# Performance work log

Measured on AMD Instinct MI355X. Metric: run time of the kernel, lower is better.

## Reference

```python
import jax, jax.numpy as jnp
import numpy as np

D = 2048
N_HEADS = 16
N_KV = 4
HEAD_DIM = D // N_HEADS  # 128
N_REP = N_HEADS // N_KV  # 4
B, S = 2, 2048


def setup_inputs() -> dict:
    key = jax.random.key(0)
    ks = jax.random.split(key, 5)
    scale = 0.02
    return {
        "x": jax.random.normal(ks[0], (B, S, D), dtype=jnp.float32),
        "wq": jax.random.normal(ks[1], (D, N_HEADS * HEAD_DIM), dtype=jnp.float32) * scale,
        "wk": jax.random.normal(ks[2], (D, N_KV * HEAD_DIM), dtype=jnp.float32) * scale,
        "wv": jax.random.normal(ks[3], (D, N_KV * HEAD_DIM), dtype=jnp.float32) * scale,
        "wo": jax.random.normal(ks[4], (N_HEADS * HEAD_DIM, D), dtype=jnp.float32) * scale,
    }


def reference(x, wq, wk, wv, wo):
    b, s, _ = x.shape
    # projections
    xq = (x @ wq).reshape(b, s, N_HEADS, HEAD_DIM)
    xk = (x @ wk).reshape(b, s, N_KV, HEAD_DIM)
    xv = (x @ wv).reshape(b, s, N_KV, HEAD_DIM)
    # GQA: group queries per kv head -> [b, n_kv, n_rep, s, d]
    xq = xq.transpose(0, 2, 1, 3).reshape(b, N_KV, N_REP, s, HEAD_DIM)
    xk = xk.transpose(0, 2, 1, 3)  # [b, n_kv, s, d]
    xv = xv.transpose(0, 2, 1, 3)
    scale = 1.0 / jnp.sqrt(jnp.asarray(HEAD_DIM, dtype=x.dtype))
    scores = jnp.einsum('bkrqd,bkvd->bkrqv', xq, xk) * scale  # [b,n_kv,n_rep,s,s]
    causal = jnp.triu(jnp.ones((s, s), dtype=bool), k=1)
    scores = jnp.where(causal, jnp.asarray(-jnp.inf, dtype=scores.dtype), scores)
    probs = jax.nn.softmax(scores, axis=-1)
    out = jnp.einsum('bkrqv,bkvd->bkrqd', probs, xv)  # [b,n_kv,n_rep,s,d]
    out = out.reshape(b, N_HEADS, s, HEAD_DIM).transpose(0, 2, 1, 3).reshape(b, s, N_HEADS * HEAD_DIM)
    return out @ wo
```

## Files before the change

kernel.cpp:

```cpp
#include <hip/hip_runtime.h>

typedef unsigned short u16;
using bf16x8 = __attribute__((ext_vector_type(8))) short;
using f32x4  = __attribute__((ext_vector_type(4))) float;

#define ATTN_NEG (-3.0e38f)

__device__ __forceinline__ u16 f2bf_rne(float f) {
  unsigned int u = __float_as_uint(f);
  u += 0x7fffu + ((u >> 16) & 1u);
  return (u16)(u >> 16);
}

__device__ __forceinline__ void load_lds16(const u16* g, u16* l) {
  using gp = const __attribute__((address_space(1))) unsigned int*;
  using lp = __attribute__((address_space(3))) unsigned int*;
  __builtin_amdgcn_global_load_lds((gp)g, (lp)l, 16, 0, 0);
}

__device__ __forceinline__ void transpose_body(const float* __restrict__ in,
                                               u16* __restrict__ out, int K, int N,
                                               int bx, int by, int tid) {
  __shared__ float tile[32][33];
  int tx = tid & 31, ty = tid >> 5;
  int x0 = bx * 32, y0 = by * 32;
  #pragma unroll
  for (int i = 0; i < 32; i += 8)
    tile[ty + i][tx] = in[(size_t)(y0 + ty + i) * N + x0 + tx];
  __syncthreads();
  #pragma unroll
  for (int i = 0; i < 32; i += 8)
    out[(size_t)(x0 + ty + i) * K + y0 + tx] = f2bf_rne(tile[tx][ty + i]);
}

__global__ __launch_bounds__(256) void prep_kernel(const float* __restrict__ x,
                                                   const float* __restrict__ wq,
                                                   const float* __restrict__ wk,
                                                   const float* __restrict__ wv,
                                                   const float* __restrict__ wo,
                                                   u16* xb, u16* wqt, u16* wkt, u16* wvt,
                                                   u16* wot) {
  int bid = blockIdx.x, tid = threadIdx.x;
  if (bid < 8192) {
    int i = bid * 1024 + tid * 4;
    float4 v = *(const float4*)(x + i);
    u16* p = xb + i;
    p[0] = f2bf_rne(v.x); p[1] = f2bf_rne(v.y); p[2] = f2bf_rne(v.z); p[3] = f2bf_rne(v.w);
  } else if (bid < 12288) {
    int t = bid - 8192;
    transpose_body(wq, wqt, 2048, 2048, t & 63, t >> 6, tid);
  } else if (bid < 13312) {
    int t = bid - 12288;
    transpose_body(wk, wkt, 2048, 512, t & 15, t >> 4, tid);
  } else if (bid < 14336) {
    int t = bid - 13312;
    transpose_body(wv, wvt, 2048, 512, t & 15, t >> 4, tid);
  } else {
    int t = bid - 14336;
    transpose_body(wo, wot, 2048, 2048, t & 63, t >> 6, tid);
  }
}

template <int MODE>
__device__ __forceinline__ void gemm_tile(const u16* __restrict__ A, const u16* __restrict__ Bt,
                                          void* __restrict__ Cv, int M, int N, int K,
                                          int bx, int by, char* smem) {
  u16* As = (u16*)smem;
  u16* Bs = (u16*)(smem + 16384);
  const int tid  = threadIdx.x;
  const int wave = tid >> 6, lane = tid & 63;
  const int quad = lane >> 4, l16 = lane & 15;
  const int m0 = by * 128, n0 = bx * 128;
  const int wm = (wave >> 1) * 64, wn = (wave & 1) * 64;
  f32x4 acc[4][4] = {};

  const int srow = lane >> 2;
  const int scol = (lane & 3) << 3;

  for (int k0 = 0; k0 < K; k0 += 64) {
    __syncthreads();
    #pragma unroll
    for (int h = 0; h < 2; ++h)
      #pragma unroll
      for (int i = 0; i < 2; ++i) {
        const int row = wave * 16 + i * 64;
        load_lds16(A  + (size_t)(m0 + row + srow) * K + k0 + h * 32 + scol,
                   As + h * 4096 + row * 32);
        load_lds16(Bt + (size_t)(n0 + row + srow) * K + k0 + h * 32 + scol,
                   Bs + h * 4096 + row * 32);
      }
    __syncthreads();
    #pragma unroll
    for (int h = 0; h < 2; ++h) {
      bf16x8 af[4], bfr[4];
      #pragma unroll
      for (int i = 0; i < 4; ++i) {
        af[i]  = *(const bf16x8*)(As + h * 4096 + (wm + i * 16 + l16) * 32 + quad * 8);
        bfr[i] = *(const bf16x8*)(Bs + h * 4096 + (wn + i * 16 + l16) * 32 + quad * 8);
      }
      #pragma unroll
      for (int mi = 0; mi < 4; ++mi)
        #pragma unroll
        for (int ni = 0; ni < 4; ++ni)
          acc[mi][ni] =
              __builtin_amdgcn_mfma_f32_16x16x32_bf16(af[mi], bfr[ni], acc[mi][ni], 0, 0, 0);
    }
  }

  if constexpr (MODE == 0 || MODE == 3) {
    const float sc = (MODE == 3) ? 0.12751742f : 1.0f;
    u16* Cb = (u16*)Cv;
    #pragma unroll
    for (int mi = 0; mi < 4; ++mi)
      #pragma unroll
      for (int ni = 0; ni < 4; ++ni) {
        int row = m0 + wm + mi * 16 + quad * 4;
        int col = n0 + wn + ni * 16 + l16;
        #pragma unroll
        for (int r = 0; r < 4; ++r)
          Cb[(size_t)(row + r) * N + col] = f2bf_rne(acc[mi][ni][r] * sc);
      }
  } else if constexpr (MODE == 1) {
    u16* Cb = (u16*)Cv;
    #pragma unroll
    for (int mi = 0; mi < 4; ++mi)
      #pragma unroll
      for (int ni = 0; ni < 4; ++ni) {
        int col = n0 + wn + ni * 16 + l16;
        #pragma unroll
        for (int r = 0; r < 4; ++r) {
          int row = m0 + wm + mi * 16 + quad * 4 + r;
          int bb = row >> 11, s = row & 2047;
          int c = s & 31;
          int cp = ((c & 15) >> 2) * 8 + ((c >> 4) & 1) * 4 + (c & 3);
          Cb[((size_t)(bb * 512 + col)) * 2048 + (s & ~31) + cp] = f2bf_rne(acc[mi][ni][r]);
        }
      }
  } else {
    float* Cf = (float*)Cv;
    #pragma unroll
    for (int mi = 0; mi < 4; ++mi)
      #pragma unroll
      for (int ni = 0; ni < 4; ++ni) {
        int row = m0 + wm + mi * 16 + quad * 4;
        int col = n0 + wn + ni * 16 + l16;
        #pragma unroll
        for (int r = 0; r < 4; ++r)
          Cf[(size_t)(row + r) * N + col] = acc[mi][ni][r];
      }
  }
}

__global__ __launch_bounds__(256) void qkv_gemm(const u16* xb, const u16* wqt, const u16* wkt,
                                                const u16* wvt, u16* Qb, u16* Kb, u16* Vt) {
  extern __shared__ char smem[];
  int bx = blockIdx.x, by = blockIdx.y;
  if (bx < 16)
    gemm_tile<3>(xb, wqt, Qb, 4096, 2048, 2048, bx, by, smem);
  else if (bx < 20)
    gemm_tile<0>(xb, wkt, Kb, 4096, 512, 2048, bx - 16, by, smem);
  else
    gemm_tile<1>(xb, wvt, Vt, 4096, 512, 2048, bx - 20, by, smem);
}

template <int MODE>
__global__ __launch_bounds__(256) void gemm_kernel(const u16* A, const u16* Bt, void* C,
                                                   int M, int N, int K) {
  extern __shared__ char smem[];
  gemm_tile<MODE>(A, Bt, C, M, N, K, blockIdx.x, blockIdx.y, smem);
}


__device__ __forceinline__ void stage_kv(const u16* __restrict__ Kg, const u16* __restrict__ Vg,
                                         int kt0, u16* __restrict__ kbuf, u16* __restrict__ vbuf,
                                         int wave, int quad, int l16) {
  #pragma unroll
  for (int i = 0; i < 4; ++i) {
    int kk = wave * 4 + i;
    load_lds16(Kg + (size_t)(kt0 + 16 * (kk & 1) + l16) * 512 + (kk >> 1) * 32 + quad * 8,
               kbuf + kk * 512);
  }
  #pragma unroll
  for (int i = 0; i < 4; ++i) {
    int f = wave * 4 + i;
    load_lds16(Vg + (size_t)(16 * f + l16) * 2048 + kt0 + quad * 8, vbuf + f * 512);
  }
}

template <bool MASKED>
__device__ __forceinline__ void attn_compute2(const u16* __restrict__ kbuf,
                                              const u16* __restrict__ vbuf,
                                              int kt0, int q0w, int quad, int l16,
                                              const bf16x8 (&qfa)[4], const bf16x8 (&qfb)[4],
                                              f32x4 (&oa)[8], f32x4 (&ob)[8],
                                              float& la, float& lb) {
  const int slot = (quad * 16 + l16) * 8;
  bf16x8 kf[8];
  #pragma unroll
  for (int kk = 0; kk < 8; ++kk) kf[kk] = *(const bf16x8*)(kbuf + kk * 512 + slot);

  f32x4 sa[2] = {}, sb[2] = {};
  #pragma unroll
  for (int h = 0; h < 2; ++h)
    #pragma unroll
    for (int ks = 0; ks < 4; ++ks) {
      sa[h] = __builtin_amdgcn_mfma_f32_16x16x32_bf16(kf[ks * 2 + h], qfa[ks], sa[h], 0, 0, 0);
      sb[h] = __builtin_amdgcn_mfma_f32_16x16x32_bf16(kf[ks * 2 + h], qfb[ks], sb[h], 0, 0, 0);
    }

  bf16x8 pca, pcb;
  #pragma unroll
  for (int h = 0; h < 2; ++h)
    #pragma unroll
    for (int r = 0; r < 4; ++r) {
      int kpos = kt0 + 16 * h + quad * 4 + r;
      float s0 = sa[h][r], s1 = sb[h][r];
      if (MASKED) {
        s0 = (kpos <= q0w + l16) ? s0 : ATTN_NEG;
        s1 = (kpos <= q0w + 16 + l16) ? s1 : ATTN_NEG;
      }
      float p0 = __builtin_amdgcn_exp2f(s0);
      float p1 = __builtin_amdgcn_exp2f(s1);
      la += p0;
      lb += p1;
      pca[h * 4 + r] = (short)f2bf_rne(p0);
      pcb[h * 4 + r] = (short)f2bf_rne(p1);
    }

  #pragma unroll
  for (int f = 0; f < 8; ++f) {
    bf16x8 v8 = *(const bf16x8*)(vbuf + f * 512 + slot);
    oa[f] = __builtin_amdgcn_mfma_f32_16x16x32_bf16(pca, v8, oa[f], 0, 0, 0);
    ob[f] = __builtin_amdgcn_mfma_f32_16x16x32_bf16(pcb, v8, ob[f], 0, 0, 0);
  }
}

__global__ __launch_bounds__(128) void attn_kernel(const u16* __restrict__ Qb,
                                                   const u16* __restrict__ Kb,
                                                   const u16* __restrict__ Vt,
                                                   u16* __restrict__ Ob) {
  constexpr int S = 2048;
  const int b = blockIdx.z, h = blockIdx.y, g = h >> 2, tp = blockIdx.x;
  const int tid = threadIdx.x;
  const int wave = tid >> 6, lane = tid & 63, quad = lane >> 4, l16 = lane & 15;
  __shared__ alignas(16) u16 Kt[2][4096];
  __shared__ alignas(16) u16 Vl[2][4096];
  __shared__ float lbuf[2][2][16];

  const u16* Kg = Kb + (size_t)b * S * 512 + g * 128;
  const u16* Vg = Vt + (size_t)(b * 512 + g * 128) * 2048;

  #pragma unroll
  for (int half = 0; half < 2; ++half) {
    const int tile = (half == 0) ? tp : 31 - tp;
    const int wrow = (half == 0) ? wave : 1 - wave;
    const int q0w = tile * 64 + wrow * 32;
    const int nsteps = 2 * tile + 2;
    const int s_diag = 2 * tile + wrow;

    bf16x8 qfa[4], qfb[4];
    const u16* qra = Qb + (size_t)(b * S + q0w + l16) * 2048 + h * 128 + quad * 8;
    const u16* qrb = qra + (size_t)16 * 2048;
    #pragma unroll
    for (int ks = 0; ks < 4; ++ks) {
      qfa[ks] = *(const bf16x8*)(qra + ks * 32);
      qfb[ks] = *(const bf16x8*)(qrb + ks * 32);
    }

    f32x4 oa[8] = {}, ob[8] = {};
    float la = 0.f, lb = 0.f;

    __syncthreads();
    stage_kv(Kg, Vg, 0, Kt[0], Vl[0], wave, quad, l16);

    for (int s = 0; s < nsteps; ++s) {
      __syncthreads();
      if (s + 1 < nsteps)
        stage_kv(Kg, Vg, (s + 1) * 32, Kt[(s + 1) & 1], Vl[(s + 1) & 1], wave, quad, l16);
      if (s < s_diag)
        attn_compute2<false>(Kt[s & 1], Vl[s & 1], s * 32, q0w, quad, l16, qfa, qfb, oa, ob,
                             la, lb);
      else if (s == s_diag)
        attn_compute2<true>(Kt[s & 1], Vl[s & 1], s * 32, q0w, quad, l16, qfa, qfb, oa, ob,
                            la, lb);
    }

    float lta = la + __shfl_xor(la, 16);
    lta += __shfl_xor(lta, 32);
    float ltb = lb + __shfl_xor(lb, 16);
    ltb += __shfl_xor(ltb, 32);
    if (quad == 0) {
      lbuf[wave][0][l16] = lta;
      lbuf[wave][1][l16] = ltb;
    }
    __builtin_amdgcn_wave_barrier();
    float ila[4], ilb[4];
    #pragma unroll
    for (int r = 0; r < 4; ++r) {
      ila[r] = 1.f / lbuf[wave][0][quad * 4 + r];
      ilb[r] = 1.f / lbuf[wave][1][quad * 4 + r];
    }

    u16* ora = Ob + (size_t)(b * S + q0w + quad * 4) * 2048 + h * 128 + l16;
    u16* orb = ora + (size_t)16 * 2048;
    #pragma unroll
    for (int f = 0; f < 8; ++f)
      #pragma unroll
      for (int r = 0; r < 4; ++r) {
        ora[(size_t)r * 2048 + f * 16] = f2bf_rne(oa[f][r] * ila[r]);
        orb[(size_t)r * 2048 + f * 16] = f2bf_rne(ob[f][r] * ilb[r]);
      }
  }
}

extern "C" void kernel_launch(void* const* d_in, const int* in_sizes, int n_in,
                              void* d_out, int out_size, void* d_ws, size_t ws_size,
                              hipStream_t stream) {
  const float* x  = (const float*)d_in[0];
  const float* wq = (const float*)d_in[1];
  const float* wk = (const float*)d_in[2];
  const float* wv = (const float*)d_in[3];
  const float* wo = (const float*)d_in[4];
  float* out = (float*)d_out;
  char* ws = (char*)d_ws;

  u16* xb  = (u16*)(ws);
  u16* wqt = (u16*)(ws + 16777216);
  u16* wkt = (u16*)(ws + 25165824);
  u16* wvt = (u16*)(ws + 27262976);
  u16* wot = (u16*)(ws + 29360128);
  u16* Qb  = (u16*)(ws + 37748736);
  u16* Kb  = (u16*)(ws + 54525952);
  u16* Vt  = (u16*)(ws + 58720256);
  u16* Ab  = (u16*)(ws + 62914560);

  prep_kernel<<<18432, 256, 0, stream>>>(x, wq, wk, wv, wo, xb, wqt, wkt, wvt, wot);
  qkv_gemm<<<dim3(24, 32), 256, 32768, stream>>>(xb, wqt, wkt, wvt, Qb, Kb, Vt);
  attn_kernel<<<dim3(16, 16, 2), 128, 0, stream>>>(Qb, Kb, Vt, Ab);
  gemm_kernel<2><<<dim3(16, 32), 256, 32768, stream>>>(Ab, wot, out, 4096, 2048, 2048);
}
```

Measured before the change: 347.5 us.

## Restructure attention into 4-wave 128-row tiles with triple-buffered KV pipeline

```diff
diff --git a/kernel.cpp b/kernel.cpp
--- a/kernel.cpp
+++ b/kernel.cpp
@@ -175,14 +175,12 @@
                                          int kt0, u16* __restrict__ kbuf, u16* __restrict__ vbuf,
                                          int wave, int quad, int l16) {
   #pragma unroll
-  for (int i = 0; i < 4; ++i) {
-    int kk = wave * 4 + i;
-    load_lds16(Kg + (size_t)(kt0 + 16 * (kk & 1) + l16) * 512 + (kk >> 1) * 32 + quad * 8,
-               kbuf + kk * 512);
-  }
-  #pragma unroll
-  for (int i = 0; i < 4; ++i) {
-    int f = wave * 4 + i;
+  for (int h = 0; h < 2; ++h)
+    load_lds16(Kg + (size_t)(kt0 + h * 16 + l16) * 512 + wave * 32 + quad * 8,
+               kbuf + (wave * 2 + h) * 512);
+  #pragma unroll
+  for (int i = 0; i < 2; ++i) {
+    int f = wave * 2 + i;
     load_lds16(Vg + (size_t)(16 * f + l16) * 2048 + kt0 + quad * 8, vbuf + f * 512);
   }
 }
@@ -200,6 +198,7 @@
   for (int kk = 0; kk < 8; ++kk) kf[kk] = *(const bf16x8*)(kbuf + kk * 512 + slot);
 
   f32x4 sa[2] = {}, sb[2] = {};
+  __builtin_amdgcn_s_setprio(1);
   #pragma unroll
   for (int h = 0; h < 2; ++h)
     #pragma unroll
@@ -207,6 +206,7 @@
       sa[h] = __builtin_amdgcn_mfma_f32_16x16x32_bf16(kf[ks * 2 + h], qfa[ks], sa[h], 0, 0, 0);
       sb[h] = __builtin_amdgcn_mfma_f32_16x16x32_bf16(kf[ks * 2 + h], qfb[ks], sb[h], 0, 0, 0);
     }
+  __builtin_amdgcn_s_setprio(0);
 
   bf16x8 pca, pcb;
   #pragma unroll
@@ -227,90 +227,98 @@
       pcb[h * 4 + r] = (short)f2bf_rne(p1);
     }
 
+  __builtin_amdgcn_s_setprio(1);
   #pragma unroll
   for (int f = 0; f < 8; ++f) {
     bf16x8 v8 = *(const bf16x8*)(vbuf + f * 512 + slot);
     oa[f] = __builtin_amdgcn_mfma_f32_16x16x32_bf16(pca, v8, oa[f], 0, 0, 0);
     ob[f] = __builtin_amdgcn_mfma_f32_16x16x32_bf16(pcb, v8, ob[f], 0, 0, 0);
   }
-}
-
-__global__ __launch_bounds__(128) void attn_kernel(const u16* __restrict__ Qb,
-                                                   const u16* __restrict__ Kb,
-                                                   const u16* __restrict__ Vt,
-                                                   u16* __restrict__ Ob) {
+  __builtin_amdgcn_s_setprio(0);
+}
+
+__global__ __launch_bounds__(256, 2) void attn_kernel(const u16* __restrict__ Qb,
+                                                      const u16* __restrict__ Kb,
+                                                      const u16* __restrict__ Vt,
+                                                      u16* __restrict__ Ob) {
   constexpr int S = 2048;
-  const int b = blockIdx.z, h = blockIdx.y, g = h >> 2, tp = blockIdx.x;
+  const int b = blockIdx.z, h = blockIdx.y, g = h >> 2;
+  const int tile = b ? blockIdx.x : (15 - blockIdx.x);
   const int tid = threadIdx.x;
   const int wave = tid >> 6, lane = tid & 63, quad = lane >> 4, l16 = lane & 15;
-  __shared__ alignas(16) u16 Kt[2][4096];
-  __shared__ alignas(16) u16 Vl[2][4096];
-  __shared__ float lbuf[2][2][16];
+  __shared__ alignas(16) u16 Kt[3][4096];
+  __shared__ alignas(16) u16 Vl[3][4096];
+  __shared__ float lbuf[4][2][16];
 
   const u16* Kg = Kb + (size_t)b * S * 512 + g * 128;
   const u16* Vg = Vt + (size_t)(b * 512 + g * 128) * 2048;
 
-  #pragma unroll
-  for (int half = 0; half < 2; ++half) {
-    const int tile = (half == 0) ? tp : 31 - tp;
-    const int wrow = (half == 0) ? wave : 1 - wave;
-    const int q0w = tile * 64 + wrow * 32;
-    const int nsteps = 2 * tile + 2;
-    const int s_diag = 2 * tile + wrow;
-
-    bf16x8 qfa[4], qfb[4];
-    const u16* qra = Qb + (size_t)(b * S + q0w + l16) * 2048 + h * 128 + quad * 8;
-    const u16* qrb = qra + (size_t)16 * 2048;
-    #pragma unroll
-    for (int ks = 0; ks < 4; ++ks) {
-      qfa[ks] = *(const bf16x8*)(qra + ks * 32);
-      qfb[ks] = *(const bf16x8*)(qrb + ks * 32);
-    }
-
-    f32x4 oa[8] = {}, ob[8] = {};
-    float la = 0.f, lb = 0.f;
-
-    __syncthreads();
-    stage_kv(Kg, Vg, 0, Kt[0], Vl[0], wave, quad, l16);
-
-    for (int s = 0; s < nsteps; ++s) {
-      __syncthreads();
-      if (s + 1 < nsteps)
-        stage_kv(Kg, Vg, (s + 1) * 32, Kt[(s + 1) & 1], Vl[(s + 1) & 1], wave, quad, l16);
-      if (s < s_diag)
-        attn_compute2<false>(Kt[s & 1], Vl[s & 1], s * 32, q0w, quad, l16, qfa, qfb, oa, ob,
-                             la, lb);
-      else if (s == s_diag)
-        attn_compute2<true>(Kt[s & 1], Vl[s & 1], s * 32, q0w, quad, l16, qfa, qfb, oa, ob,
-                            la, lb);
-    }
-
-    float lta = la + __shfl_xor(la, 16);
-    lta += __shfl_xor(lta, 32);
-    float ltb = lb + __shfl_xor(lb, 16);
-    ltb += __shfl_xor(ltb, 32);
-    if (quad == 0) {
-      lbuf[wave][0][l16] = lta;
-      lbuf[wave][1][l16] = ltb;
-    }
-    __builtin_amdgcn_wave_barrier();
-    float ila[4], ilb[4];
+  const int q0w = tile * 128 + wave * 32;
+  const int nsteps = 4 * tile + 4;
+  const int s_diag = 4 * tile + wave;
+
+  bf16x8 qfa[4], qfb[4];
+  const u16* qra = Qb + (size_t)(b * S + q0w + l16) * 2048 + h * 128 + quad * 8;
+  const u16* qrb = qra + (size_t)16 * 2048;
+  #pragma unroll
+  for (int ks = 0; ks < 4; ++ks) {
+    qfa[ks] = *(const bf16x8*)(qra + ks * 32);
+    qfb[ks] = *(const bf16x8*)(qrb + ks * 32);
+  }
+  asm volatile("s_waitcnt vmcnt(0)" ::: "memory");
+  #pragma unroll
+  for (int ks = 0; ks < 4; ++ks) {
+    asm volatile("" : "+v"(qfa[ks]));
+    asm volatile("" : "+v"(qfb[ks]));
+  }
+
+  f32x4 oa[8] = {}, ob[8] = {};
+  float la = 0.f, lb = 0.f;
+
+  stage_kv(Kg, Vg, 0, Kt[0], Vl[0], wave, quad, l16);
+  stage_kv(Kg, Vg, 32, Kt[1], Vl[1], wave, quad, l16);
+
+  for (int s = 0; s < nsteps; ++s) {
+    asm volatile("s_waitcnt vmcnt(4)" ::: "memory");
+    __builtin_amdgcn_s_barrier();
+    {
+      const int sn = (s + 2 < nsteps) ? s + 2 : nsteps - 1;
+      const int bn = (s + 2) % 3;
+      stage_kv(Kg, Vg, sn * 32, Kt[bn], Vl[bn], wave, quad, l16);
+    }
+    const int bc = s % 3;
+    if (s < s_diag)
+      attn_compute2<false>(Kt[bc], Vl[bc], s * 32, q0w, quad, l16, qfa, qfb, oa, ob, la, lb);
+    else if (s == s_diag)
+      attn_compute2<true>(Kt[bc], Vl[bc], s * 32, q0w, quad, l16, qfa, qfb, oa, ob, la, lb);
+  }
+  asm volatile("s_waitcnt vmcnt(0)" ::: "memory");
+
+  float lta = la + __shfl_xor(la, 16);
+  lta += __shfl_xor(lta, 32);
+  float ltb = lb + __shfl_xor(lb, 16);
+  ltb += __shfl_xor(ltb, 32);
+  if (quad == 0) {
+    lbuf[wave][0][l16] = lta;
+    lbuf[wave][1][l16] = ltb;
+  }
+  __builtin_amdgcn_wave_barrier();
+  float ila[4], ilb[4];
+  #pragma unroll
+  for (int r = 0; r < 4; ++r) {
+    ila[r] = 1.f / lbuf[wave][0][quad * 4 + r];
+    ilb[r] = 1.f / lbuf[wave][1][quad * 4 + r];
+  }
+
+  u16* ora = Ob + (size_t)(b * S + q0w + quad * 4) * 2048 + h * 128 + l16;
+  u16* orb = ora + (size_t)16 * 2048;
+  #pragma unroll
+  for (int f = 0; f < 8; ++f)
     #pragma unroll
     for (int r = 0; r < 4; ++r) {
-      ila[r] = 1.f / lbuf[wave][0][quad * 4 + r];
-      ilb[r] = 1.f / lbuf[wave][1][quad * 4 + r];
-    }
-
-    u16* ora = Ob + (size_t)(b * S + q0w + quad * 4) * 2048 + h * 128 + l16;
-    u16* orb = ora + (size_t)16 * 2048;
-    #pragma unroll
-    for (int f = 0; f < 8; ++f)
-      #pragma unroll
-      for (int r = 0; r < 4; ++r) {
-        ora[(size_t)r * 2048 + f * 16] = f2bf_rne(oa[f][r] * ila[r]);
-        orb[(size_t)r * 2048 + f * 16] = f2bf_rne(ob[f][r] * ilb[r]);
-      }
-  }
+      ora[(size_t)r * 2048 + f * 16] = f2bf_rne(oa[f][r] * ila[r]);
+      orb[(size_t)r * 2048 + f * 16] = f2bf_rne(ob[f][r] * ilb[r]);
+    }
 }
 
 extern "C" void kernel_launch(void* const* d_in, const int* in_sizes, int n_in,
@@ -336,6 +344,6 @@
 
   prep_kernel<<<18432, 256, 0, stream>>>(x, wq, wk, wv, wo, xb, wqt, wkt, wvt, wot);
   qkv_gemm<<<dim3(24, 32), 256, 32768, stream>>>(xb, wqt, wkt, wvt, Qb, Kb, Vt);
-  attn_kernel<<<dim3(16, 16, 2), 128, 0, stream>>>(Qb, Kb, Vt, Ab);
+  attn_kernel<<<dim3(16, 16, 2), 256, 0, stream>>>(Qb, Kb, Vt, Ab);
   gemm_kernel<2><<<dim3(16, 32), 256, 32768, stream>>>(Ab, wot, out, 4096, 2048, 2048);
 }
```

After: 311.6 us. 10.3% less time.
